# Kernel tuning notes

Measured on AMD Instinct MI355X. Metric: run time of the kernel, lower is better.

## Reference

```python
import jax, jax.numpy as jnp
import numpy as np

BETA = 0.25  # commitment loss weight (init kwarg)


def setup_inputs() -> dict:
    key = jax.random.key(0)
    k1, k2 = jax.random.split(key)
    x = jax.random.normal(k1, (64, 32, 32, 64), dtype=jnp.float32)  # [B,H,W,D]
    # keras random_uniform_initializer default: U(-0.05, 0.05)
    embeddings = jax.random.uniform(k2, (64, 512), dtype=jnp.float32,
                                    minval=-0.05, maxval=0.05)  # [D,K]
    return {"x": x, "embeddings": embeddings}


def reference(x, embeddings):
    D, K = embeddings.shape
    flat = x.reshape(-1, D)  # [N,D]
    # squared L2 distances to each code: ||f||^2 + ||e||^2 - 2 f.e  -> [N,K]
    distances = (jnp.sum(flat * flat, axis=1, keepdims=True)
                 + jnp.sum(embeddings * embeddings, axis=0)
                 - 2.0 * (flat @ embeddings))
    idx = jnp.argmin(distances, axis=1)  # [N]
    # one-hot @ embeddings^T == gather of codebook rows
    quantized = jnp.take(embeddings.T, idx, axis=0).reshape(x.shape)
    commitment_loss = BETA * jnp.mean(jnp.square(jax.lax.stop_gradient(quantized) - x))
    codebook_loss = jnp.mean(jnp.square(quantized - jax.lax.stop_gradient(x)))
    loss = commitment_loss + codebook_loss
    # straight-through estimator
    out = x + jax.lax.stop_gradient(quantized - x)
    return out, loss
```

## Files before the change

kernel.cpp:

```cpp
#include <hip/hip_runtime.h>


#define N_ROWS 65536
#define DIM 64
#define KCODES 512
#define ROWS_PER_BLOCK 128
#define THREADS 512

typedef short s16x8 __attribute__((ext_vector_type(8)));
typedef float f32x4 __attribute__((ext_vector_type(4)));

#define LOSS_OFF   0
#define EN2_OFF    256
#define EN2B_OFF   2304
#define ET_OFF     4352
#define AFR_OFF    135424

#define TAU 1.2e-3f

__device__ __forceinline__ unsigned short f2bf(float f) {
    unsigned u = __float_as_uint(f);
    return (unsigned short)((u + 0x7fffu + ((u >> 16) & 1u)) >> 16);
}
__device__ __forceinline__ float bf2f(unsigned short h) {
    return __uint_as_float(((unsigned)h) << 16);
}
__device__ __forceinline__ void cvt8(const float* __restrict__ p,
                                     s16x8& hi, s16x8& lo) {
    const float4 v0 = *(const float4*)p;
    const float4 v1 = *(const float4*)(p + 4);
    const float vv[8] = {v0.x, v0.y, v0.z, v0.w, v1.x, v1.y, v1.z, v1.w};
    #pragma unroll
    for (int j = 0; j < 8; ++j) {
        const unsigned short h = f2bf(vv[j]);
        hi[j] = (short)h;
        lo[j] = (short)f2bf(vv[j] - bf2f(h));
    }
}

__global__ void vq_prep(const float* __restrict__ emb, char* __restrict__ ws) {
    const int k = blockIdx.x * 256 + threadIdx.x;
    if (k == 0) *(double*)(ws + LOSS_OFF) = 0.0;
    float* en2  = (float*)(ws + EN2_OFF);
    float* en2b = (float*)(ws + EN2B_OFF);
    float* eT   = (float*)(ws + ET_OFF);
    uint4* Afr  = (uint4*)(ws + AFR_OFF);
    const int ctg = k >> 4, c = k & 15;
    float s = 0.0f;
    #pragma unroll
    for (int ks = 0; ks < 2; ++ks) {
        #pragma unroll
        for (int g = 0; g < 4; ++g) {
            unsigned short hb[8], lb[8];
            #pragma unroll
            for (int j = 0; j < 8; ++j) {
                const int d = ks * 32 + g * 8 + j;
                const float v = emb[d * KCODES + k];
                eT[k * DIM + d] = v;
                s = fmaf(v, v, s);
                const unsigned short h = f2bf(v);
                hb[j] = h;
                lb[j] = f2bf(v - bf2f(h));
            }
            uint4 H, L;
            H.x = hb[0] | ((unsigned)hb[1] << 16); H.y = hb[2] | ((unsigned)hb[3] << 16);
            H.z = hb[4] | ((unsigned)hb[5] << 16); H.w = hb[6] | ((unsigned)hb[7] << 16);
            L.x = lb[0] | ((unsigned)lb[1] << 16); L.y = lb[2] | ((unsigned)lb[3] << 16);
            L.z = lb[4] | ((unsigned)lb[5] << 16); L.w = lb[6] | ((unsigned)lb[7] << 16);
            const int lane = g * 16 + c;
            Afr[((ctg * 2 + ks) * 2 + 0) * 64 + lane] = H;
            Afr[((ctg * 2 + ks) * 2 + 1) * 64 + lane] = L;
        }
    }
    en2[k] = s;
    en2b[k] = s + 6.0f;
}

__global__ __launch_bounds__(THREADS, 2)
void vq_main(const float* __restrict__ x, const char* __restrict__ ws,
             float* __restrict__ out, double* __restrict__ loss_acc) {
    __shared__ unsigned long long sm_all[8][8][16];
    __shared__ unsigned pick[ROWS_PER_BLOCK];
    __shared__ unsigned char llist[ROWS_PER_BLOCK];
    __shared__ float fbuf[DIM];
    __shared__ unsigned long long wmin[8];
    __shared__ double lpart[8];
    __shared__ int lcnt;

    const int tid = threadIdx.x;
    const int bid = blockIdx.x;
    const int w = __builtin_amdgcn_readfirstlane(tid >> 6);
    const int l = tid & 63;
    if (tid == 0) lcnt = 0;

    const s16x8* Afr = (const s16x8*)(ws + AFR_OFF);
    s16x8 Aeh[4][2], Ael[4][2];
    #pragma unroll
    for (int ct = 0; ct < 4; ++ct) {
        #pragma unroll
        for (int ks = 0; ks < 2; ++ks) {
            const int ctg = w * 4 + ct;
            Aeh[ct][ks] = Afr[((ctg * 2 + ks) * 2 + 0) * 64 + l];
            Ael[ct][ks] = Afr[((ctg * 2 + ks) * 2 + 1) * 64 + l];
        }
    }
    const float* en2b = (const float*)(ws + EN2B_OFF);
    f32x4 enf[4];
    #pragma unroll
    for (int ct = 0; ct < 4; ++ct) {
        const float4 t = *(const float4*)(en2b + w * 64 + ct * 16 + (l >> 4) * 4);
        enf[ct][0] = t.x; enf[ct][1] = t.y; enf[ct][2] = t.z; enf[ct][3] = t.w;
    }
    const int codebase = w * 64 + (l >> 4) * 4;

    #pragma unroll 2
    for (int bt = 0; bt < 8; ++bt) {
        const int rowb = bid * ROWS_PER_BLOCK + bt * 16 + (l & 15);
        const float* px = x + (size_t)rowb * DIM + (l >> 4) * 8;
        s16x8 bh0, bl0, bh1, bl1;
        cvt8(px, bh0, bl0);
        cvt8(px + 32, bh1, bl1);

        unsigned m1 = 0xFFFFFFFFu, m2 = 0xFFFFFFFFu;
        #pragma unroll
        for (int ct = 0; ct < 4; ++ct) {
            f32x4 a = {0.f, 0.f, 0.f, 0.f};
            a = __builtin_amdgcn_mfma_f32_16x16x32_bf16(Aeh[ct][0], bh0, a, 0, 0, 0);
            a = __builtin_amdgcn_mfma_f32_16x16x32_bf16(Aeh[ct][1], bh1, a, 0, 0, 0);
            a = __builtin_amdgcn_mfma_f32_16x16x32_bf16(Ael[ct][0], bh0, a, 0, 0, 0);
            a = __builtin_amdgcn_mfma_f32_16x16x32_bf16(Ael[ct][1], bh1, a, 0, 0, 0);
            a = __builtin_amdgcn_mfma_f32_16x16x32_bf16(Aeh[ct][0], bl0, a, 0, 0, 0);
            a = __builtin_amdgcn_mfma_f32_16x16x32_bf16(Aeh[ct][1], bl1, a, 0, 0, 0);
            #pragma unroll
            for (int rg = 0; rg < 4; ++rg) {
                const float m = fmaf(-2.0f, a[rg], enf[ct][rg]);
                const unsigned u = (__float_as_uint(m) & 0xFFFFFE00u)
                                 | (unsigned)(codebase + ct * 16 + rg);
                const unsigned hi = m1 > u ? m1 : u;
                m1 = m1 < u ? m1 : u;
                m2 = m2 < hi ? m2 : hi;
            }
        }
        #pragma unroll
        for (int mask = 16; mask <= 32; mask <<= 1) {
            const unsigned o1 = __shfl_xor(m1, mask);
            const unsigned o2 = __shfl_xor(m2, mask);
            const unsigned hi  = m1 > o1 ? m1 : o1;
            const unsigned lo2 = m2 < o2 ? m2 : o2;
            m1 = m1 < o1 ? m1 : o1;
            m2 = hi < lo2 ? hi : lo2;
        }
        if (l < 16) sm_all[bt][w][l] = ((unsigned long long)m1 << 32) | m2;
    }
    __syncthreads();

    if (tid < ROWS_PER_BLOCK) {
        const int bt = tid >> 4, c = tid & 15;
        unsigned long long p = sm_all[bt][0][c];
        unsigned m1 = (unsigned)(p >> 32), m2 = (unsigned)p;
        #pragma unroll
        for (int w2 = 1; w2 < 8; ++w2) {
            p = sm_all[bt][w2][c];
            const unsigned a1 = (unsigned)(p >> 32), a2 = (unsigned)p;
            const unsigned hi  = m1 > a1 ? m1 : a1;
            const unsigned lo2 = m2 < a2 ? m2 : a2;
            m1 = m1 < a1 ? m1 : a1;
            m2 = hi < lo2 ? hi : lo2;
        }
        pick[tid] = m1 & 0x1FFu;
        const float f1 = __uint_as_float(m1 & 0xFFFFFE00u);
        const float f2 = __uint_as_float(m2 & 0xFFFFFE00u);
        if (f2 - f1 < TAU) {
            const int i = atomicAdd(&lcnt, 1);
            llist[i] = (unsigned char)tid;
        }
    }
    __syncthreads();

    {
        const float* eT  = (const float*)(ws + ET_OFF);
        const float* en2 = (const float*)(ws + EN2_OFF);
        const int nfb = lcnt;
        for (int i = 0; i < nfb; ++i) {
            const int r = llist[i];
            const int grow = bid * ROWS_PER_BLOCK + r;
            if (tid < 64) fbuf[tid] = x[(size_t)grow * DIM + tid];
            __syncthreads();

            const float4* fr = (const float4*)fbuf;
            float4 a4 = make_float4(0.f, 0.f, 0.f, 0.f);
            #pragma unroll
            for (int j = 0; j < 16; ++j) {
                const float4 f = fr[j];
                a4.x = fmaf(f.x, f.x, a4.x);
                a4.y = fmaf(f.y, f.y, a4.y);
                a4.z = fmaf(f.z, f.z, a4.z);
                a4.w = fmaf(f.w, f.w, a4.w);
            }
            const float r2 = (a4.x + a4.y) + (a4.z + a4.w);

            const int k = tid;
            const float4* ek = (const float4*)(eT + k * DIM);
            float4 acc4 = make_float4(0.f, 0.f, 0.f, 0.f);
            #pragma unroll
            for (int j = 0; j < 16; ++j) {
                const float4 e = ek[j];
                const float4 f = fr[j];
                acc4.x = fmaf(f.x, e.x, acc4.x);
                acc4.y = fmaf(f.y, e.y, acc4.y);
                acc4.z = fmaf(f.z, e.z, acc4.z);
                acc4.w = fmaf(f.w, e.w, acc4.w);
            }
            const float dot = (acc4.x + acc4.y) + (acc4.z + acc4.w);
            const float s = (r2 + en2[k]) - 2.0f * dot;
            unsigned long long best =
                ((unsigned long long)__float_as_uint(s) << 32) | (unsigned)k;
            #pragma unroll
            for (int mask = 1; mask <= 32; mask <<= 1) {
                const unsigned long long o = __shfl_xor(best, mask);
                if (o < best) best = o;
            }
            if (l == 0) wmin[w] = best;
            __syncthreads();
            if (tid == 0) {
                unsigned long long b = wmin[0];
                #pragma unroll
                for (int t = 1; t < 8; ++t) if (wmin[t] < b) b = wmin[t];
                pick[r] = (unsigned)(b & 0x1FFu);
            }
            __syncthreads();
        }
    }
    __syncthreads();

    {
        const float* eT = (const float*)(ws + ET_OFF);
        const int r = tid >> 2, c4 = tid & 3;
        const int grow = bid * ROWS_PER_BLOCK + r;
        const float4* xr = (const float4*)(x + (size_t)grow * DIM) + c4 * 4;
        const float4* qr = (const float4*)(eT + pick[r] * DIM) + c4 * 4;
        float4* orow = ((float4*)out) + (size_t)grow * 16 + c4 * 4;
        float lsum = 0.0f;
        #pragma unroll
        for (int j = 0; j < 4; ++j) {
            const float4 q = qr[j], xv = xr[j];
            float4 o; float dx;
            dx = q.x - xv.x; o.x = xv.x + dx; lsum = fmaf(dx, dx, lsum);
            dx = q.y - xv.y; o.y = xv.y + dx; lsum = fmaf(dx, dx, lsum);
            dx = q.z - xv.z; o.z = xv.z + dx; lsum = fmaf(dx, dx, lsum);
            dx = q.w - xv.w; o.w = xv.w + dx; lsum = fmaf(dx, dx, lsum);
            orow[j] = o;
        }
        double dl = (double)lsum;
        #pragma unroll
        for (int off = 32; off > 0; off >>= 1) dl += __shfl_down(dl, off);
        if (l == 0) lpart[w] = dl;
    }
    __syncthreads();
    if (tid == 0) {
        double s = lpart[0];
        #pragma unroll
        for (int t = 1; t < 8; ++t) s += lpart[t];
        atomicAdd(loss_acc, s);
    }
}

__global__ void vq_fin(const double* __restrict__ loss_acc, float* __restrict__ out) {
    if (threadIdx.x == 0)
        out[N_ROWS * DIM] = (float)(1.25 * loss_acc[0] * (1.0 / (double)(N_ROWS * DIM)));
}

extern "C" void kernel_launch(void* const* d_in, const int* in_sizes, int n_in,
                              void* d_out, int out_size, void* d_ws, size_t ws_size,
                              hipStream_t stream) {
    const float* x   = (const float*)d_in[0];
    const float* emb = (const float*)d_in[1];
    float* out = (float*)d_out;
    char*  ws  = (char*)d_ws;

    vq_prep<<<2, 256, 0, stream>>>(emb, ws);
    vq_main<<<N_ROWS / ROWS_PER_BLOCK, THREADS, 0, stream>>>(
        x, ws, out, (double*)(ws + LOSS_OFF));
    vq_fin<<<1, 1, 0, stream>>>((const double*)(ws + LOSS_OFF), out);
}
```

Measured before the change: 54.36 us.

## Stage x rows in LDS once and halve rows per block

Each block now loads its x rows from global memory once into shared memory. It converts them to bf16 hi/lo MFMA fragments in shared memory and reuses the staged fp32 rows for the fallback exact search and the output/loss pass, so x is no longer re-read from global memory. Rows per block drop from 128 to 64, which doubles the grid and gives each thread half as much epilogue work. LDS use rises and the block adds a barrier, which may reduce occupancy or add sync cost.

Result: faster. 50.13 us (-7.8%).

```diff
diff --git a/kernel.cpp b/kernel.cpp
--- a/kernel.cpp
+++ b/kernel.cpp
@@ -4,7 +4,7 @@
 #define N_ROWS 65536
 #define DIM 64
 #define KCODES 512
-#define ROWS_PER_BLOCK 128
+#define ROWS_PER_BLOCK 64
 #define THREADS 512
 
 typedef short s16x8 __attribute__((ext_vector_type(8)));
@@ -25,10 +25,8 @@
 __device__ __forceinline__ float bf2f(unsigned short h) {
     return __uint_as_float(((unsigned)h) << 16);
 }
-__device__ __forceinline__ void cvt8(const float* __restrict__ p,
-                                     s16x8& hi, s16x8& lo) {
-    const float4 v0 = *(const float4*)p;
-    const float4 v1 = *(const float4*)(p + 4);
+__device__ __forceinline__ void cvt8v(const float4 v0, const float4 v1,
+                                      s16x8& hi, s16x8& lo) {
     const float vv[8] = {v0.x, v0.y, v0.z, v0.w, v1.x, v1.y, v1.z, v1.w};
     #pragma unroll
     for (int j = 0; j < 8; ++j) {
@@ -79,10 +77,11 @@
 __global__ __launch_bounds__(THREADS, 2)
 void vq_main(const float* __restrict__ x, const char* __restrict__ ws,
              float* __restrict__ out, double* __restrict__ loss_acc) {
-    __shared__ unsigned long long sm_all[8][8][16];
+    __shared__ float xs[ROWS_PER_BLOCK][DIM];
+    __shared__ s16x8 Bfr[4][2][2][64];
+    __shared__ unsigned long long sm_all[4][8][16];
     __shared__ unsigned pick[ROWS_PER_BLOCK];
     __shared__ unsigned char llist[ROWS_PER_BLOCK];
-    __shared__ float fbuf[DIM];
     __shared__ unsigned long long wmin[8];
     __shared__ double lpart[8];
     __shared__ int lcnt;
@@ -93,6 +92,21 @@
     const int l = tid & 63;
     if (tid == 0) lcnt = 0;
 
+    {
+        const int r_abs = tid >> 3;
+        const int jg    = tid & 7;
+        const float* p = x + (size_t)(bid * ROWS_PER_BLOCK + r_abs) * DIM + jg * 8;
+        const float4 v0 = *(const float4*)p;
+        const float4 v1 = *(const float4*)(p + 4);
+        *(float4*)&xs[r_abs][jg * 8]     = v0;
+        *(float4*)&xs[r_abs][jg * 8 + 4] = v1;
+        s16x8 h, lo;
+        cvt8v(v0, v1, h, lo);
+        const int rt = r_abs >> 4, c = r_abs & 15;
+        Bfr[rt][jg >> 2][0][(jg & 3) * 16 + c] = h;
+        Bfr[rt][jg >> 2][1][(jg & 3) * 16 + c] = lo;
+    }
+
     const s16x8* Afr = (const s16x8*)(ws + AFR_OFF);
     s16x8 Aeh[4][2], Ael[4][2];
     #pragma unroll
@@ -113,13 +127,14 @@
     }
     const int codebase = w * 64 + (l >> 4) * 4;
 
+    __syncthreads();
+
     #pragma unroll 2
-    for (int bt = 0; bt < 8; ++bt) {
-        const int rowb = bid * ROWS_PER_BLOCK + bt * 16 + (l & 15);
-        const float* px = x + (size_t)rowb * DIM + (l >> 4) * 8;
-        s16x8 bh0, bl0, bh1, bl1;
-        cvt8(px, bh0, bl0);
-        cvt8(px + 32, bh1, bl1);
+    for (int bt = 0; bt < 4; ++bt) {
+        const s16x8 bh0 = Bfr[bt][0][0][l];
+        const s16x8 bl0 = Bfr[bt][0][1][l];
+        const s16x8 bh1 = Bfr[bt][1][0][l];
+        const s16x8 bl1 = Bfr[bt][1][1][l];
 
         unsigned m1 = 0xFFFFFFFFu, m2 = 0xFFFFFFFFu;
         #pragma unroll
@@ -183,11 +198,8 @@
         const int nfb = lcnt;
         for (int i = 0; i < nfb; ++i) {
             const int r = llist[i];
-            const int grow = bid * ROWS_PER_BLOCK + r;
-            if (tid < 64) fbuf[tid] = x[(size_t)grow * DIM + tid];
-            __syncthreads();
-
-            const float4* fr = (const float4*)fbuf;
+            const float4* fr = (const float4*)xs[r];
+
             float4 a4 = make_float4(0.f, 0.f, 0.f, 0.f);
             #pragma unroll
             for (int j = 0; j < 16; ++j) {
@@ -235,14 +247,14 @@
 
     {
         const float* eT = (const float*)(ws + ET_OFF);
-        const int r = tid >> 2, c4 = tid & 3;
+        const int r = tid >> 3, g8 = tid & 7;
         const int grow = bid * ROWS_PER_BLOCK + r;
-        const float4* xr = (const float4*)(x + (size_t)grow * DIM) + c4 * 4;
-        const float4* qr = (const float4*)(eT + pick[r] * DIM) + c4 * 4;
-        float4* orow = ((float4*)out) + (size_t)grow * 16 + c4 * 4;
+        const float4* xr = (const float4*)&xs[r][g8 * 8];
+        const float4* qr = (const float4*)(eT + pick[r] * DIM) + g8 * 2;
+        float4* orow = ((float4*)out) + (size_t)grow * 16 + g8 * 2;
         float lsum = 0.0f;
         #pragma unroll
-        for (int j = 0; j < 4; ++j) {
+        for (int j = 0; j < 2; ++j) {
             const float4 q = qr[j], xv = xr[j];
             float4 o; float dx;
             dx = q.x - xv.x; o.x = xv.x + dx; lsum = fmaf(dx, dx, lsum);
```
